# Performance work log

Hardware: AMD Instinct MI355X
Metric: run time of the kernel (lower is better)

Reference implementation:

```python
import jax, jax.numpy as jnp
import numpy as np

B, T, S, D = 32, 1024, 1024, 512
VOCAB = 1000
INSERT_TOK = jnp.array([1, 2], dtype=jnp.int64)


def setup_inputs() -> dict:
    key = jax.random.key(0)
    k1, k2, k3, k4, k5 = jax.random.split(key, 5)
    input_var = jax.random.randint(k1, (B, T), 0, VOCAB, dtype=jnp.int64)
    output = jax.random.normal(k2, (B, T, D), jnp.float32)
    context = jax.random.normal(k3, (B, S, D), jnp.float32)
    # nn.Linear(2*dim, dim): weight [D, 2D], bias [D]
    W = jax.random.normal(k4, (D, 2 * D), jnp.float32) / np.sqrt(2 * D)
    b = jax.random.normal(k5, (D,), jnp.float32) * 0.01
    return {"input_var": input_var, "output": output, "context": context,
            "di": 0, "W": W, "b": b}


def _hard_align(input_var, src_len):
    """Replicates the python double-loop: sequential 'inserted' counter per batch.
    Returns (j, valid): j[b,i] = column of the 1.0 in attn row i (torch negative
    indices wrapped), valid[b,i] = whether row i gets any 1.0 at all."""
    bsz, tgt_len = input_var.shape
    flags = jnp.isin(input_var, INSERT_TOK)  # [B,T] is token an insert token

    def step(inserted, xi):
        i, flag = xi  # i: scalar position, flag: [B]
        cond = (src_len >= i - inserted)                    # gate, per batch
        ins2 = inserted + jnp.where(cond & flag, 1, 0)      # increment before write
        j = i - ins2 - 1
        j = jnp.where(j < 0, j + src_len, j)                # torch negative-index wrap
        return ins2, (j, cond)

    idxs = jnp.arange(1, tgt_len, dtype=jnp.int32)
    init = jnp.zeros((bsz,), jnp.int32)  # init_inserted()
    _, (j_rows, valid) = jax.lax.scan(step, init, (idxs, flags[:, 1:].T))
    j_rows = j_rows.T      # [B,T-1]
    valid = valid.T        # [B,T-1]
    # row 0: attn[b,0,0] = 1.0 always
    j_full = jnp.concatenate([jnp.zeros((bsz, 1), j_rows.dtype), j_rows], axis=1)
    valid_full = jnp.concatenate([jnp.ones((bsz, 1), bool), valid], axis=1)
    return j_full, valid_full


def reference(input_var, output, context, di, W, b):
    bsz, tgt_len, hid = output.shape
    src_len = context.shape[1]
    j, valid = _hard_align(input_var, src_len)              # [B,T], [B,T]
    vf = valid[:, :, None].astype(output.dtype)
    # hard one-hot attention matrix (as the module materializes it)
    attn = jax.nn.one_hot(j, src_len, dtype=output.dtype) * vf  # [B,T,S]
    # mix = bmm(attn, context) == masked gather of context rows
    mix = jnp.take_along_axis(context, j[:, :, None].astype(jnp.int32), axis=1) * vf
    combined = jnp.concatenate([mix, output], axis=-1)      # [B,T,2D]
    out = jnp.tanh(combined @ W.T + b)                      # [B,T,D]
    return out, attn
```

## Files before the change

### kernel.cpp

```cpp
#include <hip/hip_runtime.h>
#include <hip/hip_bf16.h>

#define B_ 32
#define T_ 1024
#define S_ 1024
#define D_ 512
#define M_ (B_*T_)
#define N_ D_
#define K_ (2*D_)

typedef __attribute__((ext_vector_type(8))) short bf16x8;
typedef __attribute__((ext_vector_type(4))) float f32x4;

__device__ inline unsigned short f2bf(float x) {
    union { float f; unsigned u; } v; v.f = x;
    unsigned r = v.u + 0x7FFFu + ((v.u >> 16) & 1u);
    return (unsigned short)(r >> 16);
}

__device__ inline unsigned cvt2bf(float lo, float hi) {
#if __has_builtin(__builtin_amdgcn_cvt_pk_bf16_f32)
    typedef __attribute__((ext_vector_type(2))) __bf16 bf2;
    union { bf2 v; unsigned u; } r;
    r.v = __builtin_amdgcn_cvt_pk_bf16_f32(lo, hi);
    return r.u;
#else
    return (unsigned)f2bf(lo) | ((unsigned)f2bf(hi) << 16);
#endif
}

__device__ inline float fast_tanh(float x) {
#if __has_builtin(__builtin_amdgcn_exp2f) && __has_builtin(__builtin_amdgcn_rcpf)
    const float e = __builtin_amdgcn_exp2f(x * 2.885390082f);
    const float r = __builtin_amdgcn_rcpf(e + 1.0f);
    return 1.0f - 2.0f * r;
#else
    return tanhf(x);
#endif
}

__global__ void align_kernel(const int* __restrict__ iv, int* __restrict__ jbuf) {
    const int b = blockIdx.x;
    const int lane = threadIdx.x;
    const int* row = iv + b * T_;
    int f[16];
    int local = 0;
    const int t0 = lane * 16;
    #pragma unroll
    for (int q = 0; q < 16; ++q) {
        const int t = t0 + q;
        const int tok = row[t];
        const int fl = (t > 0 && (tok == 1 || tok == 2)) ? 1 : 0;
        f[q] = fl;
        local += fl;
    }
    int incl = local;
    #pragma unroll
    for (int off = 1; off < 64; off <<= 1) {
        const int up = __shfl_up(incl, off, 64);
        if (lane >= off) incl += up;
    }
    int run = incl - local;
    #pragma unroll
    for (int q = 0; q < 16; ++q) {
        const int t = t0 + q;
        run += f[q];
        int j;
        if (t == 0) {
            j = 0;
        } else {
            j = t - run - 1;
            if (j < 0) j += S_;
        }
        jbuf[b * T_ + t] = j;
    }
}

__global__ void pack_w(const float* __restrict__ W, unsigned short* __restrict__ Wbf) {
    const int idx = blockIdx.x * blockDim.x + threadIdx.x;
    const f32x4 a = ((const f32x4*)W)[idx * 2];
    const f32x4 c = ((const f32x4*)W)[idx * 2 + 1];
    union { bf16x8 v; unsigned u[4]; } pk;
    pk.u[0] = cvt2bf(a[0], a[1]); pk.u[1] = cvt2bf(a[2], a[3]);
    pk.u[2] = cvt2bf(c[0], c[1]); pk.u[3] = cvt2bf(c[2], c[3]);
    *(bf16x8*)(Wbf + (size_t)idx * 8) = pk.v;
}

#define BM 256
#define BN 256
#define BK 64
#define NIT (K_ / BK)
#define KMAX (K_ - BK)
#define NGEMM ((M_ / BM) * (N_ / BN))

__global__ __launch_bounds__(512, 2)
void gemm_attn(const unsigned short* __restrict__ Wbf,
               const float* __restrict__ bias,
               float* __restrict__ out,
               float* __restrict__ attn,
               const float* __restrict__ ctx,
               const float* __restrict__ outp,
               const int* __restrict__ jbuf) {
    const int bx = blockIdx.x;
    const int tid = threadIdx.x;

    __shared__ unsigned short As[2][BM * BK];
    __shared__ unsigned short Bs[2][BN * BK];

    const int lane = tid & 63;
    const int wave = tid >> 6;
    const int wm = wave >> 1, wn = wave & 1;
    const int l16 = lane & 15, quad = lane >> 4;

    const int xcd = bx & 7;
    const int bn  = (bx >> 3) & 1;
    const int bm  = ((bx >> 4) << 3) | xcd;
    const int mBase = bm * BM;
    const int nBase = bn * BN;

    const int g    = tid & 7;
    const int rsub = tid >> 3;
    const int sw   = g ^ (rsub & 7);
    const float* actx[4];
    const float* aout[4];
    const unsigned short* bSrc[4];
    #pragma unroll
    for (int it = 0; it < 4; ++it) {
        const int r = it * 64 + rsub;
        const int m = mBase + r;
        const int jm = jbuf[m];
        actx[it] = ctx + ((size_t)((m >> 10) * S_ + jm)) * D_ + g * 8;
        aout[it] = outp + (size_t)m * D_ - D_ + g * 8;
        bSrc[it] = Wbf + (size_t)(nBase + r) * K_ + sw * 8;
    }

    f32x4 acc[4][8] = {};
    f32x4 fa0[4][2], fa1[4][2];

#define LOAD_A(FA, KO) do {                                                    \
    const int _koa = (KO);                                                     \
    _Pragma("unroll")                                                          \
    for (int _it = 0; _it < 4; ++_it) {                                        \
        const float* _src = (_koa < D_) ? (actx[_it] + _koa) : (aout[_it] + _koa); \
        FA[_it][0] = ((const f32x4*)_src)[0];                                  \
        FA[_it][1] = ((const f32x4*)_src)[1];                                  \
    }                                                                          \
} while (0)

#define DMA_B(P, KO) do {                                                      \
    const int _kob = (KO);                                                     \
    _Pragma("unroll")                                                          \
    for (int _it = 0; _it < 4; ++_it) {                                        \
        __builtin_amdgcn_global_load_lds(                                      \
            (const __attribute__((address_space(1))) void*)(bSrc[_it] + _kob), \
            (__attribute__((address_space(3))) void*)(&Bs[P][(_it * 512 + tid) * 8]), \
            16, 0, 0);                                                         \
    }                                                                          \
} while (0)

#define STAGE_A(P, FA) do {                                                    \
    _Pragma("unroll")                                                          \
    for (int _it = 0; _it < 4; ++_it) {                                        \
        union { bf16x8 v; unsigned u[4]; } _pk;                                \
        _pk.u[0] = cvt2bf(FA[_it][0][0], FA[_it][0][1]);                       \
        _pk.u[1] = cvt2bf(FA[_it][0][2], FA[_it][0][3]);                       \
        _pk.u[2] = cvt2bf(FA[_it][1][0], FA[_it][1][1]);                       \
        _pk.u[3] = cvt2bf(FA[_it][1][2], FA[_it][1][3]);                       \
        *(bf16x8*)&As[P][(_it * 512 + rsub * 8 + sw) * 8] = _pk.v;             \
    }                                                                          \
} while (0)

#define MFMA_PH(P) do {                                                        \
    _Pragma("unroll")                                                          \
    for (int _ks = 0; _ks < 2; ++_ks) {                                        \
        bf16x8 _af[4], _bfr[8];                                                \
        const int _q = _ks * 4 + quad;                                         \
        _Pragma("unroll")                                                      \
        for (int _mt = 0; _mt < 4; ++_mt) {                                    \
            const int _r = wm * 64 + _mt * 16 + l16;                           \
            _af[_mt] = *(const bf16x8*)&As[P][(_r * 8 + (_q ^ (_r & 7))) * 8]; \
        }                                                                      \
        _Pragma("unroll")                                                      \
        for (int _nt = 0; _nt < 8; ++_nt) {                                    \
            const int _rb = wn * 128 + _nt * 16 + l16;                         \
            _bfr[_nt] = *(const bf16x8*)&Bs[P][(_rb * 8 + (_q ^ (_rb & 7))) * 8]; \
        }                                                                      \
        _Pragma("unroll")                                                      \
        for (int _mt = 0; _mt < 4; ++_mt)                                      \
            _Pragma("unroll")                                                  \
            for (int _nt = 0; _nt < 8; ++_nt)                                  \
                acc[_mt][_nt] = __builtin_amdgcn_mfma_f32_16x16x32_bf16(       \
                    _af[_mt], _bfr[_nt], acc[_mt][_nt], 0, 0, 0);              \
    }                                                                          \
} while (0)

    LOAD_A(fa0, 0);
    DMA_B(0, 0);
    __builtin_amdgcn_sched_barrier(0);
    LOAD_A(fa1, BK);
    __builtin_amdgcn_sched_barrier(0);
    STAGE_A(0, fa0);
    asm volatile("s_waitcnt vmcnt(8) lgkmcnt(0)" ::: "memory");
    __builtin_amdgcn_sched_barrier(0);
    __builtin_amdgcn_s_barrier();
    __builtin_amdgcn_sched_barrier(0);

    #pragma unroll 1
    for (int i = 0; i < NIT; i += 2) {
        const int ko = i * BK;
        const int k2 = (ko + 2 * BK > KMAX) ? KMAX : ko + 2 * BK;
        const int k3 = (ko + 3 * BK > KMAX) ? KMAX : ko + 3 * BK;

        DMA_B(1, ko + BK);
        __builtin_amdgcn_sched_barrier(0);
        LOAD_A(fa0, k2);
        __builtin_amdgcn_sched_barrier(0);
        STAGE_A(1, fa1);
        MFMA_PH(0);
        asm volatile("s_waitcnt vmcnt(8) lgkmcnt(0)" ::: "memory");
        __builtin_amdgcn_sched_barrier(0);
        __builtin_amdgcn_s_barrier();
        __builtin_amdgcn_sched_barrier(0);

        DMA_B(0, k2);
        __builtin_amdgcn_sched_barrier(0);
        LOAD_A(fa1, k3);
        __builtin_amdgcn_sched_barrier(0);
        STAGE_A(0, fa0);
        MFMA_PH(1);
        asm volatile("s_waitcnt vmcnt(8) lgkmcnt(0)" ::: "memory");
        __builtin_amdgcn_sched_barrier(0);
        __builtin_amdgcn_s_barrier();
        __builtin_amdgcn_sched_barrier(0);
    }

#undef LOAD_A
#undef DMA_B
#undef STAGE_A
#undef MFMA_PH

    {
        const int aBase = mBase + bn * 128;
        const int col  = tid & 255;
        const int half = tid >> 8;
        #pragma unroll 4
        for (int r = 0; r < 64; ++r) {
            const int row = aBase + r * 2 + half;
            const int j = jbuf[row];
            f32x4 v = {0.f, 0.f, 0.f, 0.f};
            if ((j >> 2) == col) v[j & 3] = 1.0f;
            __builtin_nontemporal_store(v, ((f32x4*)(attn + (size_t)row * S_)) + col);
        }
    }

    #pragma unroll
    for (int nt = 0; nt < 8; ++nt) {
        const int n = nBase + wn * 128 + nt * 16 + l16;
        const float bv = bias[n];
        #pragma unroll
        for (int mt = 0; mt < 4; ++mt) {
            #pragma unroll
            for (int r = 0; r < 4; ++r) {
                const int m = mBase + wm * 64 + mt * 16 + quad * 4 + r;
                const float val = fast_tanh(acc[mt][nt][r] + bv);
                __builtin_nontemporal_store(val, &out[(size_t)m * N_ + n]);
            }
        }
    }
}

extern "C" void kernel_launch(void* const* d_in, const int* in_sizes, int n_in,
                              void* d_out, int out_size, void* d_ws, size_t ws_size,
                              hipStream_t stream) {
    const int*   iv   = (const int*)d_in[0];
    const float* outp = (const float*)d_in[1];
    const float* ctx  = (const float*)d_in[2];
    const float* W    = (const float*)d_in[4];
    const float* bias = (const float*)d_in[5];

    float* out  = (float*)d_out;
    float* attn = out + (size_t)M_ * N_;

    int* jbuf = (int*)d_ws;
    unsigned short* Wbf = (unsigned short*)((char*)d_ws + (size_t)M_ * 4);

    align_kernel<<<B_, 64, 0, stream>>>(iv, jbuf);
    pack_w<<<(N_ * K_ / 8) / 256, 256, 0, stream>>>(W, Wbf);
    gemm_attn<<<NGEMM, 512, 0, stream>>>(Wbf, bias, out, attn, ctx, outp, jbuf);
}
```

Baseline: 370.8 us.

## Interleave attn one-hot stores into GEMM k-loop and fuse prep kernels

The alignment kernel and the weight-packing kernel become one launch with a block-index split, saving one kernel launch. Inside the GEMM, the one-hot attn rows are now written one row per wave on each k-iteration, overlapping those stores with MFMA work instead of running them as a separate tail phase. The A-operand pipeline drops from two register buffers prefetched two steps ahead to a single buffer with plain __syncthreads and no hand-placed waitcnts. This simplifies the schedule and frees registers, but leaves only one MFMA phase to hide global-load latency.

```diff
diff --git a/kernel.cpp b/kernel.cpp
--- a/kernel.cpp
+++ b/kernel.cpp
@@ -39,45 +39,48 @@
 #endif
 }
 
-__global__ void align_kernel(const int* __restrict__ iv, int* __restrict__ jbuf) {
-    const int b = blockIdx.x;
-    const int lane = threadIdx.x;
-    const int* row = iv + b * T_;
-    int f[16];
-    int local = 0;
-    const int t0 = lane * 16;
-    #pragma unroll
-    for (int q = 0; q < 16; ++q) {
-        const int t = t0 + q;
-        const int tok = row[t];
-        const int fl = (t > 0 && (tok == 1 || tok == 2)) ? 1 : 0;
-        f[q] = fl;
-        local += fl;
-    }
-    int incl = local;
-    #pragma unroll
-    for (int off = 1; off < 64; off <<= 1) {
-        const int up = __shfl_up(incl, off, 64);
-        if (lane >= off) incl += up;
-    }
-    int run = incl - local;
-    #pragma unroll
-    for (int q = 0; q < 16; ++q) {
-        const int t = t0 + q;
-        run += f[q];
-        int j;
-        if (t == 0) {
-            j = 0;
-        } else {
-            j = t - run - 1;
-            if (j < 0) j += S_;
-        }
-        jbuf[b * T_ + t] = j;
-    }
-}
-
-__global__ void pack_w(const float* __restrict__ W, unsigned short* __restrict__ Wbf) {
-    const int idx = blockIdx.x * blockDim.x + threadIdx.x;
+__global__ __launch_bounds__(256)
+void align_pack(const int* __restrict__ iv, int* __restrict__ jbuf,
+                const float* __restrict__ W, unsigned short* __restrict__ Wbf) {
+    if (blockIdx.x < 32) {
+        if (threadIdx.x >= 64) return;
+        const int b = blockIdx.x;
+        const int lane = threadIdx.x;
+        const int* row = iv + b * T_;
+        int f[16];
+        int local = 0;
+        const int t0 = lane * 16;
+        #pragma unroll
+        for (int q = 0; q < 16; ++q) {
+            const int t = t0 + q;
+            const int tok = row[t];
+            const int fl = (t > 0 && (tok == 1 || tok == 2)) ? 1 : 0;
+            f[q] = fl;
+            local += fl;
+        }
+        int incl = local;
+        #pragma unroll
+        for (int off = 1; off < 64; off <<= 1) {
+            const int up = __shfl_up(incl, off, 64);
+            if (lane >= off) incl += up;
+        }
+        int run = incl - local;
+        #pragma unroll
+        for (int q = 0; q < 16; ++q) {
+            const int t = t0 + q;
+            run += f[q];
+            int j;
+            if (t == 0) {
+                j = 0;
+            } else {
+                j = t - run - 1;
+                if (j < 0) j += S_;
+            }
+            jbuf[b * T_ + t] = j;
+        }
+        return;
+    }
+    const int idx = (blockIdx.x - 32) * 256 + threadIdx.x;
     const f32x4 a = ((const f32x4*)W)[idx * 2];
     const f32x4 c = ((const f32x4*)W)[idx * 2 + 1];
     union { bf16x8 v; unsigned u[4]; } pk;
@@ -134,16 +137,18 @@
         bSrc[it] = Wbf + (size_t)(nBase + r) * K_ + sw * 8;
     }
 
+    const int aBase = mBase + bn * 128;
+
     f32x4 acc[4][8] = {};
-    f32x4 fa0[4][2], fa1[4][2];
-
-#define LOAD_A(FA, KO) do {                                                    \
+    f32x4 fa[4][2];
+
+#define LOAD_A(KO) do {                                                        \
     const int _koa = (KO);                                                     \
     _Pragma("unroll")                                                          \
     for (int _it = 0; _it < 4; ++_it) {                                        \
         const float* _src = (_koa < D_) ? (actx[_it] + _koa) : (aout[_it] + _koa); \
-        FA[_it][0] = ((const f32x4*)_src)[0];                                  \
-        FA[_it][1] = ((const f32x4*)_src)[1];                                  \
+        fa[_it][0] = ((const f32x4*)_src)[0];                                  \
+        fa[_it][1] = ((const f32x4*)_src)[1];                                  \
     }                                                                          \
 } while (0)
 
@@ -158,16 +163,38 @@
     }                                                                          \
 } while (0)
 
-#define STAGE_A(P, FA) do {                                                    \
+#define STAGE_A(P) do {                                                        \
     _Pragma("unroll")                                                          \
     for (int _it = 0; _it < 4; ++_it) {                                        \
         union { bf16x8 v; unsigned u[4]; } _pk;                                \
-        _pk.u[0] = cvt2bf(FA[_it][0][0], FA[_it][0][1]);                       \
-        _pk.u[1] = cvt2bf(FA[_it][0][2], FA[_it][0][3]);                       \
-        _pk.u[2] = cvt2bf(FA[_it][1][0], FA[_it][1][1]);                       \
-        _pk.u[3] = cvt2bf(FA[_it][1][2], FA[_it][1][3]);                       \
+        _pk.u[0] = cvt2bf(fa[_it][0][0], fa[_it][0][1]);                       \
+        _pk.u[1] = cvt2bf(fa[_it][0][2], fa[_it][0][3]);                       \
+        _pk.u[2] = cvt2bf(fa[_it][1][0], fa[_it][1][1]);                       \
+        _pk.u[3] = cvt2bf(fa[_it][1][2], fa[_it][1][3]);                       \
         *(bf16x8*)&As[P][(_it * 512 + rsub * 8 + sw) * 8] = _pk.v;             \
     }                                                                          \
+} while (0)
+
+#define FLY_UNDER(I, PN) do {                                                  \
+                  \
+    {                                                                          \
+        const int _arow = aBase + (I) * 8 + wave;        \
+        const int _jv = jbuf[_arow];                     \
+        f32x4* _ab = (f32x4*)(attn + (size_t)_arow * S_);                      \
+        _Pragma("unroll")                                                      \
+        for (int _s = 0; _s < 4; ++_s) {                                       \
+            const int _col = lane + 64 * _s;                                   \
+            f32x4 _v = {0.f, 0.f, 0.f, 0.f};                                   \
+            if ((_jv >> 2) == _col) _v[_jv & 3] = 1.0f;                        \
+            __builtin_nontemporal_store(_v, _ab + _col);                       \
+        }                                                                      \
+    }                                                                          \
+    {                                                                          \
+        const int _kon = ((I) * BK + BK > KMAX) ? KMAX : (I) * BK + BK;        \
+        LOAD_A(_kon);                                              \
+        DMA_B(PN, _kon);                                  \
+    }                                                                          \
+    __builtin_amdgcn_sched_barrier(0);                    \
 } while (0)
 
 #define MFMA_PH(P) do {                                                        \
@@ -194,64 +221,27 @@
     }                                                                          \
 } while (0)
 
-    LOAD_A(fa0, 0);
+    LOAD_A(0);
     DMA_B(0, 0);
-    __builtin_amdgcn_sched_barrier(0);
-    LOAD_A(fa1, BK);
-    __builtin_amdgcn_sched_barrier(0);
-    STAGE_A(0, fa0);
-    asm volatile("s_waitcnt vmcnt(8) lgkmcnt(0)" ::: "memory");
-    __builtin_amdgcn_sched_barrier(0);
-    __builtin_amdgcn_s_barrier();
-    __builtin_amdgcn_sched_barrier(0);
 
     #pragma unroll 1
     for (int i = 0; i < NIT; i += 2) {
-        const int ko = i * BK;
-        const int k2 = (ko + 2 * BK > KMAX) ? KMAX : ko + 2 * BK;
-        const int k3 = (ko + 3 * BK > KMAX) ? KMAX : ko + 3 * BK;
-
-        DMA_B(1, ko + BK);
-        __builtin_amdgcn_sched_barrier(0);
-        LOAD_A(fa0, k2);
-        __builtin_amdgcn_sched_barrier(0);
-        STAGE_A(1, fa1);
+        STAGE_A(0);
+        __syncthreads();
+        FLY_UNDER(i, 1);
         MFMA_PH(0);
-        asm volatile("s_waitcnt vmcnt(8) lgkmcnt(0)" ::: "memory");
-        __builtin_amdgcn_sched_barrier(0);
-        __builtin_amdgcn_s_barrier();
-        __builtin_amdgcn_sched_barrier(0);
-
-        DMA_B(0, k2);
-        __builtin_amdgcn_sched_barrier(0);
-        LOAD_A(fa1, k3);
-        __builtin_amdgcn_sched_barrier(0);
-        STAGE_A(0, fa0);
+
+        STAGE_A(1);
+        __syncthreads();
+        FLY_UNDER(i + 1, 0);
         MFMA_PH(1);
-        asm volatile("s_waitcnt vmcnt(8) lgkmcnt(0)" ::: "memory");
-        __builtin_amdgcn_sched_barrier(0);
-        __builtin_amdgcn_s_barrier();
-        __builtin_amdgcn_sched_barrier(0);
     }
 
 #undef LOAD_A
 #undef DMA_B
 #undef STAGE_A
+#undef FLY_UNDER
 #undef MFMA_PH
-
-    {
-        const int aBase = mBase + bn * 128;
-        const int col  = tid & 255;
-        const int half = tid >> 8;
-        #pragma unroll 4
-        for (int r = 0; r < 64; ++r) {
-            const int row = aBase + r * 2 + half;
-            const int j = jbuf[row];
-            f32x4 v = {0.f, 0.f, 0.f, 0.f};
-            if ((j >> 2) == col) v[j & 3] = 1.0f;
-            __builtin_nontemporal_store(v, ((f32x4*)(attn + (size_t)row * S_)) + col);
-        }
-    }
 
     #pragma unroll
     for (int nt = 0; nt < 8; ++nt) {
@@ -284,7 +274,6 @@
     int* jbuf = (int*)d_ws;
     unsigned short* Wbf = (unsigned short*)((char*)d_ws + (size_t)M_ * 4);
 
-    align_kernel<<<B_, 64, 0, stream>>>(iv, jbuf);
-    pack_w<<<(N_ * K_ / 8) / 256, 256, 0, stream>>>(W, Wbf);
+    align_pack<<<32 + (N_ * K_ / 8) / 256, 256, 0, stream>>>(iv, jbuf, W, Wbf);
     gemm_attn<<<NGEMM, 512, 0, stream>>>(Wbf, bias, out, attn, ctx, outp, jbuf);
 }
```

Measured after the change: 367.3 us. No clear change (-0.9%).
